# Performance work log

Hardware: AMD Instinct MI355X
Metric: run time of the kernel (lower is better)

Reference implementation:

```python
import jax, jax.numpy as jnp
import numpy as np

NUM_NODES = 20000
NUM_EDGES = 320000
NODE_DIM = 256
EDGE_DIM = 64
HIDDEN = 512

def _glorot(key, shape):
    fan_in = shape[0]
    bound = 1.0 / np.sqrt(fan_in)
    return jax.random.uniform(key, shape, jnp.float32, -bound, bound)

def setup_inputs() -> dict:
    key = jax.random.key(0)
    ks = jax.random.split(key, 12)
    node_features = jax.random.normal(ks[0], (NUM_NODES, NODE_DIM), jnp.float32)
    edge_index = jax.random.randint(ks[1], (2, NUM_EDGES), 0, NUM_NODES, jnp.int64 if jax.config.jax_enable_x64 else jnp.int32)
    edge_features = jax.random.normal(ks[2], (NUM_EDGES, EDGE_DIM), jnp.float32)
    edge_in = 2 * NODE_DIM + EDGE_DIM
    node_in = NODE_DIM + HIDDEN
    params = {
        'W1': _glorot(ks[3], (edge_in, HIDDEN)), 'b1': _glorot(ks[4], (HIDDEN,)),
        'W2': _glorot(ks[5], (HIDDEN, HIDDEN)), 'b2': _glorot(ks[6], (HIDDEN,)),
        'W3': _glorot(ks[7], (node_in, HIDDEN)), 'b3': _glorot(ks[8], (HIDDEN,)),
        'W4': _glorot(ks[9], (HIDDEN, NODE_DIM)), 'b4': _glorot(ks[10], (NODE_DIM,)),
    }
    return {'node_features': node_features, 'edge_index': edge_index,
            'edge_features': edge_features, **params}

def reference(node_features, edge_index, edge_features,
              W1, b1, W2, b2, W3, b3, W4, b4):
    src_idx = edge_index[0]
    tgt_idx = edge_index[1]
    # gather endpoints: [E, 2*node_dim + edge_dim]
    edge_input = jnp.concatenate(
        [node_features[src_idx], node_features[tgt_idx], edge_features], axis=-1)
    # edge MLP
    h = jax.nn.relu(edge_input @ W1 + b1)
    messages = h @ W2 + b2                      # [E, hidden]
    # scatter-add aggregate per target node
    aggregated = jax.ops.segment_sum(messages, tgt_idx, num_segments=NUM_NODES)
    # node MLP + residual
    node_input = jnp.concatenate([node_features, aggregated], axis=-1)
    g = jax.nn.relu(node_input @ W3 + b3)
    node_update = g @ W4 + b4                   # [N, node_dim]
    return node_features + node_update
```

## Files before the change

### kernel.cpp

```cpp
#include <hip/hip_runtime.h>

#define NUM_NODES 20000
#define NUM_EDGES 320000
#define NODE_DIM  256
#define EDGE_DIM  64
#define HIDDEN    512

typedef short  s16x8  __attribute__((ext_vector_type(8)));
typedef float  f32x16 __attribute__((ext_vector_type(16)));
typedef unsigned short us16;

__device__ __forceinline__ us16 f2bf(float f) {
    union { float f; unsigned u; } c; c.f = f;
    unsigned r = c.u + 0x7fffu + ((c.u >> 16) & 1u);
    return (us16)(r >> 16);
}
__device__ __forceinline__ float bf2f(us16 b) {
    union { unsigned u; float f; } c; c.u = ((unsigned)b) << 16;
    return c.f;
}
__device__ __forceinline__ int swapmid(int x) {
    return (x & 3) | ((x & 4) << 1) | ((x & 8) >> 1);
}
__device__ __forceinline__ void zero16(f32x16& a) {
    #pragma unroll
    for (int i = 0; i < 16; ++i) a[i] = 0.0f;
}
__device__ __forceinline__ void mfma3(f32x16& acc, s16x8 ah, s16x8 al, s16x8 bh, s16x8 bl) {
    acc = __builtin_amdgcn_mfma_f32_32x32x16_bf16(ah, bh, acc, 0, 0, 0);
    acc = __builtin_amdgcn_mfma_f32_32x32x16_bf16(ah, bl, acc, 0, 0, 0);
    acc = __builtin_amdgcn_mfma_f32_32x32x16_bf16(al, bh, acc, 0, 0, 0);
}
template<int STRIDE>
__device__ __forceinline__ void stash_quad(char* hi, char* lo, int r, int c, float4 v) {
    int cpp = (c & ~15) | swapmid(c & 15);
    int off = r * STRIDE + ((cpp * 2) ^ ((r & 7) << 4));
    us16 h0 = f2bf(v.x), h1 = f2bf(v.y), h2 = f2bf(v.z), h3 = f2bf(v.w);
    uint2 uh; uh.x = h0 | ((unsigned)h1 << 16); uh.y = h2 | ((unsigned)h3 << 16);
    uint2 ul;
    ul.x = f2bf(v.x - bf2f(h0)) | ((unsigned)f2bf(v.y - bf2f(h1)) << 16);
    ul.y = f2bf(v.z - bf2f(h2)) | ((unsigned)f2bf(v.w - bf2f(h3)) << 16);
    *reinterpret_cast<uint2*>(hi + off) = uh;
    *reinterpret_cast<uint2*>(lo + off) = ul;
}
template<int STRIDE>
__device__ __forceinline__ void bread(const char* hi, const char* lo, int r, int kbyte,
                                      s16x8& bh, s16x8& bl) {
    int off = r * STRIDE + (kbyte ^ ((r & 7) << 4));
    bh = *reinterpret_cast<const s16x8*>(hi + off);
    bl = *reinterpret_cast<const s16x8*>(lo + off);
}

__global__ void build_deg(const int* __restrict__ tgt, int* __restrict__ deg) {
    int i = blockIdx.x * 256 + threadIdx.x;
    if (i < NUM_EDGES) atomicAdd(&deg[tgt[i]], 1);
}

__global__ void scan_deg(const int* __restrict__ deg, int* __restrict__ off) {
    __shared__ int buf[1024];
    __shared__ int carry;
    int tid = threadIdx.x;
    if (tid == 0) { carry = 0; off[0] = 0; }
    __syncthreads();
    for (int base = 0; base < NUM_NODES; base += 1024) {
        int v = (base + tid < NUM_NODES) ? deg[base + tid] : 0;
        buf[tid] = v; __syncthreads();
        for (int d = 1; d < 1024; d <<= 1) {
            int add = (tid >= d) ? buf[tid - d] : 0;
            __syncthreads();
            buf[tid] += add;
            __syncthreads();
        }
        int inc = buf[tid] + carry;
        if (base + tid < NUM_NODES) off[base + tid + 1] = inc;
        __syncthreads();
        if (tid == 1023) carry = inc;
        __syncthreads();
    }
}

__global__ void fill_csr(const int* __restrict__ tgt, const int* __restrict__ off,
                         int* __restrict__ cursor, int* __restrict__ csr) {
    int i = blockIdx.x * 256 + threadIdx.x;
    if (i < NUM_EDGES) {
        int t = tgt[i];
        int p = atomicAdd(&cursor[t], 1);
        csr[off[t] + p] = i;
    }
}

__global__ void compute_w23(const float* __restrict__ W2, const float* __restrict__ b2,
                            const float* __restrict__ W3,
                            float* __restrict__ W23, float* __restrict__ b23) {
    int n = blockIdx.y * 256 + threadIdx.x;
    int i = blockIdx.x;
    const float* w3b = W3 + 256 * 512 + n;
    float s = 0.f;
    if (i < 512) {
        const float* w2r = W2 + i * 512;
        for (int j = 0; j < 512; ++j) s = fmaf(w2r[j], w3b[(size_t)j * 512], s);
        W23[i * 512 + n] = s;
    } else {
        for (int j = 0; j < 512; ++j) s = fmaf(b2[j], w3b[(size_t)j * 512], s);
        b23[n] = s;
    }
}

__global__ void prep_planes(const float* __restrict__ W1, const float* __restrict__ W3,
                            const float* __restrict__ W4, const float* __restrict__ W23,
                            us16* __restrict__ wab_h, us16* __restrict__ wab_l,
                            us16* __restrict__ wc_h,  us16* __restrict__ wc_l,
                            us16* __restrict__ w34_h, us16* __restrict__ w34_l,
                            us16* __restrict__ w4_h,  us16* __restrict__ w4_l) {
    int idx = blockIdx.x * 256 + threadIdx.x;
    float w; us16 *dh, *dl; int k, n, N;
    if (idx < 262144) {
        n = idx & 1023; k = idx >> 10; N = 1024;
        w = W1[(k + (n >= 512 ? 256 : 0)) * 512 + (n & 511)];
        dh = wab_h; dl = wab_l;
    } else if (idx < 294912) {
        int j = idx - 262144; n = j & 511; k = j >> 9; N = 512;
        w = W1[(512 + k) * 512 + n];
        dh = wc_h; dl = wc_l;
    } else if (idx < 688128) {
        int j = idx - 294912; n = j & 511; k = j >> 9; N = 512;
        w = (k < 256) ? W3[k * 512 + n] : W23[(k - 256) * 512 + n];
        dh = w34_h; dl = w34_l;
    } else {
        int j = idx - 688128; n = j & 255; k = j >> 8; N = 256;
        w = W4[k * 256 + n];
        dh = w4_h; dl = w4_l;
    }
    us16 h = f2bf(w);
    us16 l = f2bf(w - bf2f(h));
    int d = (k >> 4) * (N * 16) + n * 16 + swapmid(k & 15);
    dh[d] = h; dl[d] = l;
}

__global__ __launch_bounds__(512, 2)
void gemm_p(const float* __restrict__ nf,
            const us16* __restrict__ wab_h, const us16* __restrict__ wab_l,
            float* __restrict__ P) {
    __shared__ char sB[32768];
    const int tid = threadIdx.x;
    const int nb  = blockIdx.x * 32;
    const int half = blockIdx.y;

    const float4* nf4 = reinterpret_cast<const float4*>(nf);
    for (int i = tid; i < 32 * 64; i += 512) {
        int r = i >> 6, q = i & 63;
        stash_quad<512>(sB, sB + 16384, r, 4 * q, nf4[(size_t)(nb + r) * 64 + q]);
    }
    __syncthreads();

    const int w = tid >> 6, l = tid & 63, le = l & 31, g = l >> 5;
    const s16x8* Ah = reinterpret_cast<const s16x8*>(wab_h);
    const s16x8* Al = reinterpret_cast<const s16x8*>(wab_l);
    const int nbase = half * 512 + w * 64;

    f32x16 acc[2]; zero16(acc[0]); zero16(acc[1]);
    for (int ks = 0; ks < 16; ++ks) {
        s16x8 AH[2], AL[2], bh, bl;
        #pragma unroll
        for (int mt = 0; mt < 2; ++mt) {
            int idx = ks * 2048 + (nbase + 32 * mt + le) * 2 + g;
            AH[mt] = Ah[idx]; AL[mt] = Al[idx];
        }
        bread<512>(sB, sB + 16384, le, ks * 32 + 16 * g, bh, bl);
        #pragma unroll
        for (int mt = 0; mt < 2; ++mt) mfma3(acc[mt], AH[mt], AL[mt], bh, bl);
    }

    float4* P4 = reinterpret_cast<float4*>(P);
    #pragma unroll
    for (int mt = 0; mt < 2; ++mt)
        #pragma unroll
        for (int rq = 0; rq < 4; ++rq) {
            int nn = nbase + 32 * mt + 4 * g + 8 * rq;
            float4 o = make_float4(acc[mt][4*rq+0], acc[mt][4*rq+1],
                                   acc[mt][4*rq+2], acc[mt][4*rq+3]);
            P4[(size_t)(nb + le) * 256 + (nn >> 2)] = o;
        }
}

__global__ __launch_bounds__(512, 2)
void edge_csr(const float* __restrict__ ef,
              const int* __restrict__ srcI, const int* __restrict__ tgtI,
              const int* __restrict__ csr,
              const us16* __restrict__ wc_h, const us16* __restrict__ wc_l,
              const float* __restrict__ b1, const float* __restrict__ P,
              float* __restrict__ aggH) {
    __shared__ char sB[16384];
    __shared__ int sEid[64], sSrc[64], sTgt[64];

    const int tid  = threadIdx.x;
    const int orig = blockIdx.x;
    const int wg   = (orig & 7) * 625 + (orig >> 3);
    const int cb   = wg * 64;

    if (tid < 64) {
        int eid = csr[cb + tid];
        sEid[tid] = eid; sSrc[tid] = srcI[eid]; sTgt[tid] = tgtI[eid];
    }
    __syncthreads();

    const float4* ef4 = reinterpret_cast<const float4*>(ef);
    for (int i = tid; i < 64 * 16; i += 512) {
        int e = i >> 4, q = i & 15;
        stash_quad<128>(sB, sB + 8192, e, 4 * q, ef4[(size_t)sEid[e] * 16 + q]);
    }
    __syncthreads();

    const int w = tid >> 6, l = tid & 63, le = l & 31, g = l >> 5;
    const s16x8* Ah = reinterpret_cast<const s16x8*>(wc_h);
    const s16x8* Al = reinterpret_cast<const s16x8*>(wc_l);

    f32x16 acc[2][2];
    #pragma unroll
    for (int mt = 0; mt < 2; ++mt) { zero16(acc[mt][0]); zero16(acc[mt][1]); }

    for (int ks = 0; ks < 4; ++ks) {
        s16x8 AH[2], AL[2], bh[2], bl[2];
        #pragma unroll
        for (int mt = 0; mt < 2; ++mt) {
            int idx = ks * 1024 + (w * 64 + 32 * mt + le) * 2 + g;
            AH[mt] = Ah[idx]; AL[mt] = Al[idx];
        }
        #pragma unroll
        for (int nt = 0; nt < 2; ++nt)
            bread<128>(sB, sB + 8192, 32 * nt + le, ks * 32 + 16 * g, bh[nt], bl[nt]);
        #pragma unroll
        for (int mt = 0; mt < 2; ++mt)
            #pragma unroll
            for (int nt = 0; nt < 2; ++nt)
                mfma3(acc[mt][nt], AH[mt], AL[mt], bh[nt], bl[nt]);
    }

    const float4* P4  = reinterpret_cast<const float4*>(P);
    const float4* b14 = reinterpret_cast<const float4*>(b1);

    #pragma unroll
    for (int nt = 0; nt < 2; ++nt) {
        const int es = 32 * nt + le;
        const int t = sTgt[es], s = sSrc[es];
        int tp = __shfl_up(t, 1, 32);
        const bool head = (le == 0) || (tp != t);
        bool eq[5];
        #pragma unroll
        for (int d = 0; d < 5; ++d) {
            int td = __shfl_down(t, 1 << d, 32);
            eq[d] = (le + (1 << d) < 32) && (td == t);
        }
        #pragma unroll
        for (int mt = 0; mt < 2; ++mt) {
            float4 ps[4], pt[4];
            #pragma unroll
            for (int rq = 0; rq < 4; ++rq) {
                const int h0 = w * 64 + 32 * mt + 4 * g + 8 * rq;
                ps[rq] = P4[(size_t)s * 256 + (h0 >> 2)];
                pt[rq] = P4[(size_t)t * 256 + 128 + (h0 >> 2)];
            }
            #pragma unroll
            for (int rq = 0; rq < 4; ++rq) {
                const int h0 = w * 64 + 32 * mt + 4 * g + 8 * rq;
                float4 bq = b14[h0 >> 2];
                float v0 = fmaxf(acc[mt][nt][4*rq+0] + ps[rq].x + pt[rq].x + bq.x, 0.f);
                float v1 = fmaxf(acc[mt][nt][4*rq+1] + ps[rq].y + pt[rq].y + bq.y, 0.f);
                float v2 = fmaxf(acc[mt][nt][4*rq+2] + ps[rq].z + pt[rq].z + bq.z, 0.f);
                float v3 = fmaxf(acc[mt][nt][4*rq+3] + ps[rq].w + pt[rq].w + bq.w, 0.f);
                #pragma unroll
                for (int d = 0; d < 5; ++d) {
                    float o0 = __shfl_down(v0, 1 << d, 32);
                    float o1 = __shfl_down(v1, 1 << d, 32);
                    float o2 = __shfl_down(v2, 1 << d, 32);
                    float o3 = __shfl_down(v3, 1 << d, 32);
                    if (eq[d]) { v0 += o0; v1 += o1; v2 += o2; v3 += o3; }
                }
                if (head) {
                    float* dst = aggH + (size_t)t * 512 + h0;
                    atomicAdd(dst + 0, v0); atomicAdd(dst + 1, v1);
                    atomicAdd(dst + 2, v2); atomicAdd(dst + 3, v3);
                }
            }
        }
    }
}

__global__ __launch_bounds__(512, 1)
void node_mlp(const float* __restrict__ nf, const float* __restrict__ aggH,
              const int* __restrict__ deg,
              const us16* __restrict__ w34_h, const us16* __restrict__ w34_l,
              const us16* __restrict__ w4_h,  const us16* __restrict__ w4_l,
              const float* __restrict__ b3, const float* __restrict__ b23,
              const float* __restrict__ b4, float* __restrict__ out) {
    extern __shared__ char sm[];
    __shared__ int sDeg[32];
    const int tid = threadIdx.x;
    const int nb  = blockIdx.x * 32;

    if (tid < 32) sDeg[tid] = deg[nb + tid];

    const float4* nf4 = reinterpret_cast<const float4*>(nf);
    const float4* ag4 = reinterpret_cast<const float4*>(aggH);
    for (int i = tid; i < 32 * 64; i += 512) {
        int r = i >> 6, q = i & 63;
        stash_quad<1536>(sm, sm + 49152, r, 4 * q, nf4[(size_t)(nb + r) * 64 + q]);
    }
    for (int i = tid; i < 32 * 128; i += 512) {
        int r = i >> 7, q = i & 127;
        stash_quad<1536>(sm, sm + 49152, r, 256 + 4 * q, ag4[(size_t)(nb + r) * 128 + q]);
    }
    __syncthreads();

    const int w = tid >> 6, l = tid & 63, le = l & 31, g = l >> 5;

    f32x16 acc[2]; zero16(acc[0]); zero16(acc[1]);
    {
        const s16x8* Ah = reinterpret_cast<const s16x8*>(w34_h);
        const s16x8* Al = reinterpret_cast<const s16x8*>(w34_l);
        for (int ks = 0; ks < 48; ++ks) {
            s16x8 AH[2], AL[2], bh, bl;
            #pragma unroll
            for (int mt = 0; mt < 2; ++mt) {
                int idx = ks * 1024 + (w * 64 + 32 * mt + le) * 2 + g;
                AH[mt] = Ah[idx]; AL[mt] = Al[idx];
            }
            bread<1536>(sm, sm + 49152, le, ks * 32 + 16 * g, bh, bl);
            #pragma unroll
            for (int mt = 0; mt < 2; ++mt) mfma3(acc[mt], AH[mt], AL[mt], bh, bl);
        }
    }
    __syncthreads();

    {
        const float4* b34  = reinterpret_cast<const float4*>(b3);
        const float4* b234 = reinterpret_cast<const float4*>(b23);
        const float degv = (float)sDeg[le];
        #pragma unroll
        for (int mt = 0; mt < 2; ++mt)
            #pragma unroll
            for (int rq = 0; rq < 4; ++rq) {
                int hcol = w * 64 + 32 * mt + 4 * g + 8 * rq;
                float4 bq = b34[hcol >> 2], cq = b234[hcol >> 2];
                float4 gv;
                gv.x = fmaxf(acc[mt][4*rq+0] + bq.x + degv * cq.x, 0.f);
                gv.y = fmaxf(acc[mt][4*rq+1] + bq.y + degv * cq.y, 0.f);
                gv.z = fmaxf(acc[mt][4*rq+2] + bq.z + degv * cq.z, 0.f);
                gv.w = fmaxf(acc[mt][4*rq+3] + bq.w + degv * cq.w, 0.f);
                stash_quad<1024>(sm, sm + 32768, le, hcol, gv);
            }
    }
    __syncthreads();

    f32x16 a2; zero16(a2);
    {
        const s16x8* Ah = reinterpret_cast<const s16x8*>(w4_h);
        const s16x8* Al = reinterpret_cast<const s16x8*>(w4_l);
        for (int ks = 0; ks < 32; ++ks) {
            s16x8 AH, AL, bh, bl;
            int idx = ks * 512 + (w * 32 + le) * 2 + g;
            AH = Ah[idx]; AL = Al[idx];
            bread<1024>(sm, sm + 32768, le, ks * 32 + 16 * g, bh, bl);
            mfma3(a2, AH, AL, bh, bl);
        }
    }

    const float4* b44 = reinterpret_cast<const float4*>(b4);
    float4* out4 = reinterpret_cast<float4*>(out);
    #pragma unroll
    for (int rq = 0; rq < 4; ++rq) {
        int n0 = w * 32 + 4 * g + 8 * rq;
        float4 bq  = b44[n0 >> 2];
        float4 res = nf4[(size_t)(nb + le) * 64 + (n0 >> 2)];
        float4 o;
        o.x = res.x + a2[4*rq+0] + bq.x;
        o.y = res.y + a2[4*rq+1] + bq.y;
        o.z = res.z + a2[4*rq+2] + bq.z;
        o.w = res.w + a2[4*rq+3] + bq.w;
        out4[(size_t)(nb + le) * 64 + (n0 >> 2)] = o;
    }
}

extern "C" void kernel_launch(void* const* d_in, const int* in_sizes, int n_in,
                              void* d_out, int out_size, void* d_ws, size_t ws_size,
                              hipStream_t stream) {
    const float* nf = (const float*)d_in[0];
    const int*   ei = (const int*)d_in[1];
    const float* ef = (const float*)d_in[2];
    const float* W1 = (const float*)d_in[3];
    const float* b1 = (const float*)d_in[4];
    const float* W2 = (const float*)d_in[5];
    const float* b2 = (const float*)d_in[6];
    const float* W3 = (const float*)d_in[7];
    const float* b3 = (const float*)d_in[8];
    const float* W4 = (const float*)d_in[9];
    const float* b4 = (const float*)d_in[10];
    float* out = (float*)d_out;

    char* ws = (char*)d_ws;
    float* P      = (float*)(ws + 0);
    float* aggH   = (float*)(ws + 81920000);
    us16*  wab_h  = (us16*)(ws + 122880000);
    us16*  wab_l  = (us16*)(ws + 123404288);
    us16*  wc_h   = (us16*)(ws + 123928576);
    us16*  wc_l   = (us16*)(ws + 123994112);
    us16*  w34_h  = (us16*)(ws + 124059648);
    us16*  w34_l  = (us16*)(ws + 124846080);
    us16*  w4_h   = (us16*)(ws + 125632512);
    us16*  w4_l   = (us16*)(ws + 125894656);
    float* W23    = (float*)(ws + 126156800);
    float* b23    = (float*)(ws + 127205376);
    int*   deg    = (int*)  (ws + 127207424);
    int*   cursor = (int*)  (ws + 127287424);
    int*   offs   = (int*)  (ws + 127367424);
    int*   csr    = (int*)  (ws + 127447440);

    const int* src = ei;
    const int* tgt = ei + NUM_EDGES;

    (void)hipFuncSetAttribute(reinterpret_cast<const void*>(&node_mlp),
                              hipFuncAttributeMaxDynamicSharedMemorySize, 98304);

    hipMemsetAsync(deg, 0, 160000, stream);
    hipMemsetAsync(aggH, 0, (size_t)NUM_NODES * HIDDEN * 4, stream);

    build_deg<<<1250, 256, 0, stream>>>(tgt, deg);
    scan_deg<<<1, 1024, 0, stream>>>(deg, offs);
    fill_csr<<<1250, 256, 0, stream>>>(tgt, offs, cursor, csr);

    compute_w23<<<dim3(513, 2), 256, 0, stream>>>(W2, b2, W3, W23, b23);
    prep_planes<<<3200, 256, 0, stream>>>(W1, W3, W4, W23,
                                          wab_h, wab_l, wc_h, wc_l,
                                          w34_h, w34_l, w4_h, w4_l);

    gemm_p<<<dim3(625, 2), 512, 0, stream>>>(nf, wab_h, wab_l, P);
    edge_csr<<<5000, 512, 0, stream>>>(ef, src, tgt, csr, wc_h, wc_l, b1, P, aggH);
    node_mlp<<<625, 512, 98304, stream>>>(nf, aggH, deg, w34_h, w34_l,
                                          w4_h, w4_l, b3, b23, b4, out);
}
```

Measured before the change: 933.8 us.

## Retile P GEMM, restructure edge aggregation via LDS, double-buffer node MLP staging

gemm_p now processes 64 node rows per block, so each loaded weight fragment feeds twice as many MFMAs, with clamped loads and guarded stores for the tail. edge_csr processes edges in two halves of 32, writes the edge-feature GEMM result to swizzled LDS, and then accumulates per-target sums sequentially per column slice, replacing the shuffle-based segmented reduction. node_mlp stages its input in three chunks with double-buffered LDS, cutting shared memory from 96KB to 64KB so two blocks fit per CU. The changes trade register and LDS pressure and extra barriers for more reuse and occupancy. They also risk worse atomic contention patterns.

```diff
diff --git a/kernel.cpp b/kernel.cpp
--- a/kernel.cpp
+++ b/kernel.cpp
@@ -141,15 +141,16 @@
 void gemm_p(const float* __restrict__ nf,
             const us16* __restrict__ wab_h, const us16* __restrict__ wab_l,
             float* __restrict__ P) {
-    __shared__ char sB[32768];
+    extern __shared__ char sB[];
     const int tid = threadIdx.x;
-    const int nb  = blockIdx.x * 32;
+    const int nb  = blockIdx.x * 64;
     const int half = blockIdx.y;
 
     const float4* nf4 = reinterpret_cast<const float4*>(nf);
-    for (int i = tid; i < 32 * 64; i += 512) {
+    for (int i = tid; i < 64 * 64; i += 512) {
         int r = i >> 6, q = i & 63;
-        stash_quad<512>(sB, sB + 16384, r, 4 * q, nf4[(size_t)(nb + r) * 64 + q]);
+        int row = nb + r; if (row >= NUM_NODES) row = NUM_NODES - 1;
+        stash_quad<512>(sB, sB + 32768, r, 4 * q, nf4[(size_t)row * 64 + q]);
     }
     __syncthreads();
 
@@ -158,39 +159,54 @@
     const s16x8* Al = reinterpret_cast<const s16x8*>(wab_l);
     const int nbase = half * 512 + w * 64;
 
-    f32x16 acc[2]; zero16(acc[0]); zero16(acc[1]);
+    f32x16 acc[2][2];
+    #pragma unroll
+    for (int a = 0; a < 2; ++a) { zero16(acc[a][0]); zero16(acc[a][1]); }
+
     for (int ks = 0; ks < 16; ++ks) {
-        s16x8 AH[2], AL[2], bh, bl;
+        s16x8 AH[2], AL[2], bh[2], bl[2];
         #pragma unroll
         for (int mt = 0; mt < 2; ++mt) {
             int idx = ks * 2048 + (nbase + 32 * mt + le) * 2 + g;
             AH[mt] = Ah[idx]; AL[mt] = Al[idx];
         }
-        bread<512>(sB, sB + 16384, le, ks * 32 + 16 * g, bh, bl);
-        #pragma unroll
-        for (int mt = 0; mt < 2; ++mt) mfma3(acc[mt], AH[mt], AL[mt], bh, bl);
+        #pragma unroll
+        for (int rt = 0; rt < 2; ++rt)
+            bread<512>(sB, sB + 32768, 32 * rt + le, ks * 32 + 16 * g, bh[rt], bl[rt]);
+        #pragma unroll
+        for (int mt = 0; mt < 2; ++mt)
+            #pragma unroll
+            for (int rt = 0; rt < 2; ++rt)
+                mfma3(acc[mt][rt], AH[mt], AL[mt], bh[rt], bl[rt]);
     }
 
     float4* P4 = reinterpret_cast<float4*>(P);
     #pragma unroll
-    for (int mt = 0; mt < 2; ++mt)
-        #pragma unroll
-        for (int rq = 0; rq < 4; ++rq) {
-            int nn = nbase + 32 * mt + 4 * g + 8 * rq;
-            float4 o = make_float4(acc[mt][4*rq+0], acc[mt][4*rq+1],
-                                   acc[mt][4*rq+2], acc[mt][4*rq+3]);
-            P4[(size_t)(nb + le) * 256 + (nn >> 2)] = o;
-        }
+    for (int rt = 0; rt < 2; ++rt) {
+        int row = nb + 32 * rt + le;
+        if (row < NUM_NODES) {
+            #pragma unroll
+            for (int mt = 0; mt < 2; ++mt)
+                #pragma unroll
+                for (int rq = 0; rq < 4; ++rq) {
+                    int nn = nbase + 32 * mt + 4 * g + 8 * rq;
+                    float4 o = make_float4(acc[mt][rt][4*rq+0], acc[mt][rt][4*rq+1],
+                                           acc[mt][rt][4*rq+2], acc[mt][rt][4*rq+3]);
+                    P4[(size_t)row * 256 + (nn >> 2)] = o;
+                }
+        }
+    }
 }
 
 __global__ __launch_bounds__(512, 2)
-void edge_csr(const float* __restrict__ ef,
-              const int* __restrict__ srcI, const int* __restrict__ tgtI,
-              const int* __restrict__ csr,
+void edge_csr(const int* __restrict__ srcI, const int* __restrict__ tgtI,
+              const int* __restrict__ csr, const float* __restrict__ ef,
               const us16* __restrict__ wc_h, const us16* __restrict__ wc_l,
               const float* __restrict__ b1, const float* __restrict__ P,
               float* __restrict__ aggH) {
-    __shared__ char sB[16384];
+    extern __shared__ char dsm[];
+    char* sC = dsm;
+    char* sB = dsm + 65536;
     __shared__ int sEid[64], sSrc[64], sTgt[64];
 
     const int tid  = threadIdx.x;
@@ -205,88 +221,78 @@
     __syncthreads();
 
     const float4* ef4 = reinterpret_cast<const float4*>(ef);
-    for (int i = tid; i < 64 * 16; i += 512) {
-        int e = i >> 4, q = i & 15;
-        stash_quad<128>(sB, sB + 8192, e, 4 * q, ef4[(size_t)sEid[e] * 16 + q]);
-    }
-    __syncthreads();
-
+    const float4* P4  = reinterpret_cast<const float4*>(P);
+    const float4* b14 = reinterpret_cast<const float4*>(b1);
     const int w = tid >> 6, l = tid & 63, le = l & 31, g = l >> 5;
     const s16x8* Ah = reinterpret_cast<const s16x8*>(wc_h);
     const s16x8* Al = reinterpret_cast<const s16x8*>(wc_l);
 
-    f32x16 acc[2][2];
     #pragma unroll
-    for (int mt = 0; mt < 2; ++mt) { zero16(acc[mt][0]); zero16(acc[mt][1]); }
-
-    for (int ks = 0; ks < 4; ++ks) {
-        s16x8 AH[2], AL[2], bh[2], bl[2];
+    for (int half = 0; half < 2; ++half) {
+        {
+            int e = tid >> 4, q = tid & 15;
+            stash_quad<128>(sB, sB + 4096, e, 4 * q,
+                            ef4[(size_t)sEid[half * 32 + e] * 16 + q]);
+        }
+        __syncthreads();
+
         #pragma unroll
         for (int mt = 0; mt < 2; ++mt) {
-            int idx = ks * 1024 + (w * 64 + 32 * mt + le) * 2 + g;
-            AH[mt] = Ah[idx]; AL[mt] = Al[idx];
-        }
-        #pragma unroll
-        for (int nt = 0; nt < 2; ++nt)
-            bread<128>(sB, sB + 8192, 32 * nt + le, ks * 32 + 16 * g, bh[nt], bl[nt]);
-        #pragma unroll
-        for (int mt = 0; mt < 2; ++mt)
-            #pragma unroll
-            for (int nt = 0; nt < 2; ++nt)
-                mfma3(acc[mt][nt], AH[mt], AL[mt], bh[nt], bl[nt]);
-    }
-
-    const float4* P4  = reinterpret_cast<const float4*>(P);
-    const float4* b14 = reinterpret_cast<const float4*>(b1);
-
-    #pragma unroll
-    for (int nt = 0; nt < 2; ++nt) {
-        const int es = 32 * nt + le;
-        const int t = sTgt[es], s = sSrc[es];
-        int tp = __shfl_up(t, 1, 32);
-        const bool head = (le == 0) || (tp != t);
-        bool eq[5];
-        #pragma unroll
-        for (int d = 0; d < 5; ++d) {
-            int td = __shfl_down(t, 1 << d, 32);
-            eq[d] = (le + (1 << d) < 32) && (td == t);
-        }
-        #pragma unroll
-        for (int mt = 0; mt < 2; ++mt) {
-            float4 ps[4], pt[4];
+            f32x16 acc; zero16(acc);
+            #pragma unroll
+            for (int ks = 0; ks < 4; ++ks) {
+                int idx = ks * 1024 + (w * 64 + 32 * mt + le) * 2 + g;
+                s16x8 bh, bl;
+                bread<128>(sB, sB + 4096, le, ks * 32 + 16 * g, bh, bl);
+                mfma3(acc, Ah[idx], Al[idx], bh, bl);
+            }
             #pragma unroll
             for (int rq = 0; rq < 4; ++rq) {
-                const int h0 = w * 64 + 32 * mt + 4 * g + 8 * rq;
-                ps[rq] = P4[(size_t)s * 256 + (h0 >> 2)];
-                pt[rq] = P4[(size_t)t * 256 + 128 + (h0 >> 2)];
+                int h0 = w * 64 + 32 * mt + 4 * g + 8 * rq;
+                float4 bq = b14[h0 >> 2];
+                float4 v = make_float4(acc[4*rq+0] + bq.x, acc[4*rq+1] + bq.y,
+                                       acc[4*rq+2] + bq.z, acc[4*rq+3] + bq.w);
+                *reinterpret_cast<float4*>(sC + le * 2048 + ((h0 * 4) ^ ((le & 15) << 4))) = v;
             }
-            #pragma unroll
-            for (int rq = 0; rq < 4; ++rq) {
-                const int h0 = w * 64 + 32 * mt + 4 * g + 8 * rq;
-                float4 bq = b14[h0 >> 2];
-                float v0 = fmaxf(acc[mt][nt][4*rq+0] + ps[rq].x + pt[rq].x + bq.x, 0.f);
-                float v1 = fmaxf(acc[mt][nt][4*rq+1] + ps[rq].y + pt[rq].y + bq.y, 0.f);
-                float v2 = fmaxf(acc[mt][nt][4*rq+2] + ps[rq].z + pt[rq].z + bq.z, 0.f);
-                float v3 = fmaxf(acc[mt][nt][4*rq+3] + ps[rq].w + pt[rq].w + bq.w, 0.f);
-                #pragma unroll
-                for (int d = 0; d < 5; ++d) {
-                    float o0 = __shfl_down(v0, 1 << d, 32);
-                    float o1 = __shfl_down(v1, 1 << d, 32);
-                    float o2 = __shfl_down(v2, 1 << d, 32);
-                    float o3 = __shfl_down(v3, 1 << d, 32);
-                    if (eq[d]) { v0 += o0; v1 += o1; v2 += o2; v3 += o3; }
+        }
+        __syncthreads();
+
+        {
+            const int slice = tid & 127;
+            const int e0    = half * 32 + (tid >> 7) * 8;
+            float4 sum = make_float4(0.f, 0.f, 0.f, 0.f);
+            int tcur = sTgt[e0];
+            float4 pt = P4[(size_t)tcur * 256 + 128 + slice];
+            #pragma unroll
+            for (int i = 0; i < 8; ++i) {
+                int eg = e0 + i;
+                int t = sTgt[eg];
+                if (t != tcur) {
+                    float* d = aggH + (size_t)tcur * 512 + slice * 4;
+                    atomicAdd(d + 0, sum.x); atomicAdd(d + 1, sum.y);
+                    atomicAdd(d + 2, sum.z); atomicAdd(d + 3, sum.w);
+                    sum = make_float4(0.f, 0.f, 0.f, 0.f);
+                    tcur = t;
+                    pt = P4[(size_t)t * 256 + 128 + slice];
                 }
-                if (head) {
-                    float* dst = aggH + (size_t)t * 512 + h0;
-                    atomicAdd(dst + 0, v0); atomicAdd(dst + 1, v1);
-                    atomicAdd(dst + 2, v2); atomicAdd(dst + 3, v3);
-                }
+                float4 pa = P4[(size_t)sSrc[eg] * 256 + slice];
+                int crow = eg & 31;
+                float4 c = *reinterpret_cast<const float4*>(
+                    sC + crow * 2048 + ((slice * 16) ^ ((crow & 15) << 4)));
+                sum.x += fmaxf(pa.x + pt.x + c.x, 0.f);
+                sum.y += fmaxf(pa.y + pt.y + c.y, 0.f);
+                sum.z += fmaxf(pa.z + pt.z + c.z, 0.f);
+                sum.w += fmaxf(pa.w + pt.w + c.w, 0.f);
             }
-        }
-    }
-}
-
-__global__ __launch_bounds__(512, 1)
+            float* d = aggH + (size_t)tcur * 512 + slice * 4;
+            atomicAdd(d + 0, sum.x); atomicAdd(d + 1, sum.y);
+            atomicAdd(d + 2, sum.z); atomicAdd(d + 3, sum.w);
+        }
+        __syncthreads();
+    }
+}
+
+__global__ __launch_bounds__(512, 2)
 void node_mlp(const float* __restrict__ nf, const float* __restrict__ aggH,
               const int* __restrict__ deg,
               const us16* __restrict__ w34_h, const us16* __restrict__ w34_l,
@@ -302,14 +308,16 @@
 
     const float4* nf4 = reinterpret_cast<const float4*>(nf);
     const float4* ag4 = reinterpret_cast<const float4*>(aggH);
-    for (int i = tid; i < 32 * 64; i += 512) {
-        int r = i >> 6, q = i & 63;
-        stash_quad<1536>(sm, sm + 49152, r, 4 * q, nf4[(size_t)(nb + r) * 64 + q]);
-    }
-    for (int i = tid; i < 32 * 128; i += 512) {
-        int r = i >> 7, q = i & 127;
-        stash_quad<1536>(sm, sm + 49152, r, 256 + 4 * q, ag4[(size_t)(nb + r) * 128 + q]);
-    }
+    auto stage = [&](int c, char* buf) {
+        for (int i = tid; i < 32 * 64; i += 512) {
+            int r = i >> 6, q = i & 63;
+            float4 v = (c == 0) ? nf4[(size_t)(nb + r) * 64 + q]
+                                : ag4[(size_t)(nb + r) * 128 + (c - 1) * 64 + q];
+            stash_quad<512>(buf, buf + 16384, r, 4 * q, v);
+        }
+    };
+
+    stage(0, sm);
     __syncthreads();
 
     const int w = tid >> 6, l = tid & 63, le = l & 31, g = l >> 5;
@@ -318,19 +326,27 @@
     {
         const s16x8* Ah = reinterpret_cast<const s16x8*>(w34_h);
         const s16x8* Al = reinterpret_cast<const s16x8*>(w34_l);
-        for (int ks = 0; ks < 48; ++ks) {
-            s16x8 AH[2], AL[2], bh, bl;
-            #pragma unroll
-            for (int mt = 0; mt < 2; ++mt) {
-                int idx = ks * 1024 + (w * 64 + 32 * mt + le) * 2 + g;
-                AH[mt] = Ah[idx]; AL[mt] = Al[idx];
+        #pragma unroll
+        for (int c = 0; c < 3; ++c) {
+            char* cur = sm + (c & 1) * 32768;
+            char* oth = sm + ((c + 1) & 1) * 32768;
+            if (c < 2) stage(c + 1, oth);
+            #pragma unroll
+            for (int ksl = 0; ksl < 16; ++ksl) {
+                int ks = c * 16 + ksl;
+                s16x8 AH[2], AL[2], bh, bl;
+                #pragma unroll
+                for (int mt = 0; mt < 2; ++mt) {
+                    int idx = ks * 1024 + (w * 64 + 32 * mt + le) * 2 + g;
+                    AH[mt] = Ah[idx]; AL[mt] = Al[idx];
+                }
+                bread<512>(cur, cur + 16384, le, ksl * 32 + 16 * g, bh, bl);
+                #pragma unroll
+                for (int mt = 0; mt < 2; ++mt) mfma3(acc[mt], AH[mt], AL[mt], bh, bl);
             }
-            bread<1536>(sm, sm + 49152, le, ks * 32 + 16 * g, bh, bl);
-            #pragma unroll
-            for (int mt = 0; mt < 2; ++mt) mfma3(acc[mt], AH[mt], AL[mt], bh, bl);
-        }
-    }
-    __syncthreads();
+            __syncthreads();
+        }
+    }
 
     {
         const float4* b34  = reinterpret_cast<const float4*>(b3);
@@ -418,8 +434,12 @@
     const int* src = ei;
     const int* tgt = ei + NUM_EDGES;
 
+    (void)hipFuncSetAttribute(reinterpret_cast<const void*>(&edge_csr),
+                              hipFuncAttributeMaxDynamicSharedMemorySize, 73728);
     (void)hipFuncSetAttribute(reinterpret_cast<const void*>(&node_mlp),
-                              hipFuncAttributeMaxDynamicSharedMemorySize, 98304);
+                              hipFuncAttributeMaxDynamicSharedMemorySize, 65536);
+    (void)hipFuncSetAttribute(reinterpret_cast<const void*>(&gemm_p),
+                              hipFuncAttributeMaxDynamicSharedMemorySize, 65536);
 
     hipMemsetAsync(deg, 0, 160000, stream);
     hipMemsetAsync(aggH, 0, (size_t)NUM_NODES * HIDDEN * 4, stream);
@@ -433,8 +453,8 @@
                                           wab_h, wab_l, wc_h, wc_l,
                                           w34_h, w34_l, w4_h, w4_l);
 
-    gemm_p<<<dim3(625, 2), 512, 0, stream>>>(nf, wab_h, wab_l, P);
-    edge_csr<<<5000, 512, 0, stream>>>(ef, src, tgt, csr, wc_h, wc_l, b1, P, aggH);
-    node_mlp<<<625, 512, 98304, stream>>>(nf, aggH, deg, w34_h, w34_l,
+    gemm_p<<<dim3(313, 2), 512, 65536, stream>>>(nf, wab_h, wab_l, P);
+    edge_csr<<<5000, 512, 73728, stream>>>(src, tgt, csr, ef, wc_h, wc_l, b1, P, aggH);
+    node_mlp<<<625, 512, 65536, stream>>>(nf, aggH, deg, w34_h, w34_l,
                                           w4_h, w4_l, b3, b23, b4, out);
 }
```

New measurement: 821.6 us. -12.0%, faster.
